# Kernel optimization log

Measured on AMD Instinct MI355X. Metric: run time of the kernel, lower is better.

## Reference

```python
import jax, jax.numpy as jnp
import numpy as np

N_EMBD = 1024
N_HEAD = 16  # per-source: this becomes the per-head DIM after the quirky view
B, T = 1, 2048


def setup_inputs() -> dict:
    key = jax.random.key(0)
    ks = jax.random.split(key, 5)
    s = 1.0 / np.sqrt(N_EMBD)
    x = jax.random.normal(ks[0], (B, T, N_EMBD), dtype=jnp.float32)
    attn_mask = jnp.ones((T, T), dtype=bool)
    W_qkv = jax.random.normal(ks[1], (N_EMBD, 3 * N_EMBD), dtype=jnp.float32) * s
    b_qkv = jnp.zeros((3 * N_EMBD,), dtype=jnp.float32)
    W_out = jax.random.normal(ks[2], (N_EMBD, N_EMBD), dtype=jnp.float32) * s
    b_out = jnp.zeros((N_EMBD,), dtype=jnp.float32)
    return {"x": x, "attn_mask": attn_mask, "W_qkv": W_qkv, "b_qkv": b_qkv,
            "W_out": W_out, "b_out": b_out}


def reference(x, attn_mask, W_qkv, b_qkv, W_out, b_out):
    Bb, Tt, C = x.shape
    H = N_HEAD            # per-head dim (source's layout quirk)
    nh = C // H           # number of heads = 64
    qkv = x @ W_qkv + b_qkv                      # [B,T,3C]
    q, k, v = jnp.split(qkv, 3, axis=-1)

    def to_heads(t):
        return t.reshape(Bb, Tt, nh, H).transpose(0, 2, 1, 3)  # [B,nh,T,H]

    q, k, v = to_heads(q), to_heads(k), to_heads(v)
    scale = 1.0 / np.sqrt(H)
    scores = jnp.einsum('bhqd,bhkd->bhqk', q, k) * scale       # [B,nh,T,T]
    causal = jnp.tril(jnp.ones((Tt, Tt), dtype=bool))
    scores = jnp.where(causal, scores, jnp.finfo(scores.dtype).min)
    p = jax.nn.softmax(scores, axis=-1)
    attn = jnp.einsum('bhqk,bhkd->bhqd', p, v)                 # [B,nh,T,H]
    attn = attn.transpose(0, 2, 1, 3).reshape(Bb, Tt, C)       # [B,T,C]
    return attn @ W_out + b_out
```

## Files before the change

kernel.cpp:

```cpp
#include <hip/hip_runtime.h>
#include <math.h>

#define T_SEQ 2048
#define C_EMB 1024
#define NH 64
#define HD 16

typedef __attribute__((ext_vector_type(4))) float    floatx4;
typedef __attribute__((ext_vector_type(4))) _Float16 halfx4;
typedef __attribute__((ext_vector_type(8))) _Float16 halfx8;

#if __has_builtin(__builtin_amdgcn_exp2f)
#define EXP2F(x) __builtin_amdgcn_exp2f(x)
#else
#define EXP2F(x) exp2f(x)
#endif

__device__ __forceinline__ void load_lds16(const void* g, void* l) {
    __builtin_amdgcn_global_load_lds(
        (const __attribute__((address_space(1))) unsigned int*)g,
        (__attribute__((address_space(3))) unsigned int*)l, 16, 0, 0);
}

__global__ __launch_bounds__(256) void prep_kernel(
    const float* __restrict__ x, const float* __restrict__ W_qkv,
    const float* __restrict__ W_out,
    _Float16* __restrict__ xb, _Float16* __restrict__ wqkvt,
    _Float16* __restrict__ woutt)
{
    __shared__ float s[32][33];
    const int b = blockIdx.x;
    const int t = threadIdx.x;

    if (b < 2048) {
        const int i = b * 256 + t;
        float4 v = ((const float4*)x)[i];
        halfx4 o = { (_Float16)v.x, (_Float16)v.y, (_Float16)v.z, (_Float16)v.w };
        ((halfx4*)xb)[i] = o;
        return;
    }

    const float* W; _Float16* Wt; int Kdim, Ndim, n0, k0;
    if (b < 5120) {
        const int bb = b - 2048;
        W = W_qkv; Wt = wqkvt; Kdim = 1024; Ndim = 3072;
        n0 = (bb % 96) * 32; k0 = (bb / 96) * 32;
    } else {
        const int bb = b - 5120;
        W = W_out; Wt = woutt; Kdim = 1024; Ndim = 1024;
        n0 = (bb & 31) * 32; k0 = (bb >> 5) * 32;
    }
    const int r  = t >> 3;
    const int c4 = (t & 7) * 4;
    float4 v = *(const float4*)&W[(size_t)(k0 + r) * Ndim + n0 + c4];
    s[r][c4 + 0] = v.x; s[r][c4 + 1] = v.y; s[r][c4 + 2] = v.z; s[r][c4 + 3] = v.w;
    __syncthreads();
    halfx4 o = { (_Float16)s[c4 + 0][r], (_Float16)s[c4 + 1][r],
                 (_Float16)s[c4 + 2][r], (_Float16)s[c4 + 3][r] };
    *(halfx4*)&Wt[(size_t)(n0 + r) * Kdim + k0 + c4] = o;
}

template <bool OUT_F16>
__global__ __launch_bounds__(256) void gemm_mfma_kernel(
    const _Float16* __restrict__ A,
    const _Float16* __restrict__ Bt,
    const float* __restrict__ bias,
    void* __restrict__ Cout,
    int M, int N, int K)
{
    __shared__ _Float16 As[2][64 * 32];
    __shared__ _Float16 Bs[2][128 * 32];

    const int tid = threadIdx.x;
    const int lane = tid & 63;
    const int w = tid >> 6;
    const int row0 = blockIdx.y * 64;
    const int col0 = blockIdx.x * 128;

    floatx4 acc[4][2] = {};

    const int lrow = lane >> 2;
    const int lko  = (lane & 3) * 8;
    const _Float16* agp = A  + (size_t)(row0 + w * 16 + lrow) * K + lko;
    const _Float16* bgp = Bt + (size_t)(col0 + w * 32 + lrow) * K + lko;
    const size_t rstep = (size_t)16 * K;

    const int kfr = (lane >> 4) * 8;
    const int fm = lane & 15;

    for (int k0 = 0; k0 < K; k0 += 64) {
#pragma unroll
        for (int s = 0; s < 2; ++s) {
            const int kk = k0 + s * 32;
            load_lds16(agp + kk,         &As[s][(w * 16) * 32]);
            load_lds16(bgp + kk,         &Bs[s][(w * 32) * 32]);
            load_lds16(bgp + kk + rstep, &Bs[s][(w * 32 + 16) * 32]);
        }
        __syncthreads();

#pragma unroll
        for (int s = 0; s < 2; ++s) {
            halfx8 af[4], bfv[2];
#pragma unroll
            for (int mi = 0; mi < 4; ++mi)
                af[mi] = *(const halfx8*)(&As[s][(mi * 16 + fm) * 32 + kfr]);
#pragma unroll
            for (int ni = 0; ni < 2; ++ni)
                bfv[ni] = *(const halfx8*)(&Bs[s][(w * 32 + ni * 16 + fm) * 32 + kfr]);

#pragma unroll
            for (int mi = 0; mi < 4; ++mi)
#pragma unroll
                for (int ni = 0; ni < 2; ++ni)
                    acc[mi][ni] = __builtin_amdgcn_mfma_f32_16x16x32_f16(
                        af[mi], bfv[ni], acc[mi][ni], 0, 0, 0);
        }
        __syncthreads();
    }

#pragma unroll
    for (int mi = 0; mi < 4; ++mi) {
        const int rm = row0 + mi * 16 + (lane >> 4) * 4;
#pragma unroll
        for (int ni = 0; ni < 2; ++ni) {
            const int cn = col0 + w * 32 + ni * 16 + fm;
            const float bv = bias[cn];
#pragma unroll
            for (int r = 0; r < 4; ++r) {
                float val = acc[mi][ni][r] + bv;
                if (OUT_F16)
                    ((_Float16*)Cout)[(size_t)(rm + r) * N + cn] = (_Float16)val;
                else
                    ((float*)Cout)[(size_t)(rm + r) * N + cn] = val;
            }
        }
    }
}

__global__ __launch_bounds__(512) void attn_mfma_kernel(
    const _Float16* __restrict__ qkv,
    _Float16* __restrict__ out)
{
    __shared__ _Float16 Ks[128 * 20];
    __shared__ _Float16 Vt[16 * 132];

    const int tid  = threadIdx.x;
    const int lane = tid & 63;
    const int w    = tid >> 6;
    const int quad = lane >> 4;
    const int ql   = lane & 15;
    const int h    = blockIdx.y;
    const int p    = blockIdx.x;

    const int q0s[2] = { p * 128 + w * 16, (15 - p) * 128 + w * 16 };
    const int nkt    = 16 - p;

    const _Float16 qscale = (_Float16)0.36067376f;
    halfx4 qf[2];
#pragma unroll
    for (int sub = 0; sub < 2; ++sub) {
        halfx4 qv = *(const halfx4*)(qkv + (size_t)(q0s[sub] + ql) * (3 * C_EMB)
                                     + h * HD + quad * 4);
#pragma unroll
        for (int j = 0; j < 4; ++j) qf[sub][j] = qv[j] * qscale;
    }

    const halfx4 onesA = { (_Float16)1.f, (_Float16)1.f, (_Float16)1.f, (_Float16)1.f };
    floatx4 o[2]  = {};
    floatx4 ol[2] = {};

    const int skp = tid >> 2;
    const int sdg = (tid & 3) * 4;

    for (int kt = 0; kt < nkt; ++kt) {
        const int kbase = kt * 128;
        {
            const _Float16* kp = qkv + (size_t)(kbase + skp) * (3 * C_EMB)
                                 + C_EMB + h * HD + sdg;
            *(halfx4*)&Ks[skp * 20 + sdg] = *(const halfx4*)kp;
            halfx4 vv = *(const halfx4*)(kp + C_EMB);
#pragma unroll
            for (int i = 0; i < 4; ++i) Vt[(sdg + i) * 132 + skp] = vv[i];
        }
        __syncthreads();

        halfx4 kf[8], vf[8];
#pragma unroll
        for (int st = 0; st < 8; ++st) {
            kf[st] = *(const halfx4*)&Ks[(st * 16 + ql) * 20 + quad * 4];
            vf[st] = *(const halfx4*)&Vt[ql * 132 + st * 16 + quad * 4];
        }

#pragma unroll
        for (int sub = 0; sub < 2; ++sub) {
            if (kbase > q0s[sub] + 15) continue;
            const bool need_mask = (kbase + 127 > q0s[sub]);

#pragma unroll
            for (int st = 0; st < 8; ++st) {
                floatx4 s = __builtin_amdgcn_mfma_f32_16x16x16f16(
                    kf[st], qf[sub], (floatx4){0.f, 0.f, 0.f, 0.f}, 0, 0, 0);
                if (need_mask) {
                    const int kg = kbase + st * 16 + quad * 4;
                    const int qg = q0s[sub] + ql;
#pragma unroll
                    for (int r = 0; r < 4; ++r)
                        if (kg + r > qg) s[r] = -INFINITY;
                }
                halfx4 pf;
#pragma unroll
                for (int r = 0; r < 4; ++r) pf[r] = (_Float16)EXP2F(s[r]);
                o[sub]  = __builtin_amdgcn_mfma_f32_16x16x16f16(
                    vf[st], pf, o[sub], 0, 0, 0);
                ol[sub] = __builtin_amdgcn_mfma_f32_16x16x16f16(
                    onesA, pf, ol[sub], 0, 0, 0);
            }
        }
        __syncthreads();
    }

#pragma unroll
    for (int sub = 0; sub < 2; ++sub) {
        const float inv_l = 1.f / ol[sub][0];
        halfx4 ov;
#pragma unroll
        for (int r = 0; r < 4; ++r) ov[r] = (_Float16)(o[sub][r] * inv_l);
        *(halfx4*)&out[(size_t)(q0s[sub] + ql) * C_EMB + h * HD + quad * 4] = ov;
    }
}

extern "C" void kernel_launch(void* const* d_in, const int* in_sizes, int n_in,
                              void* d_out, int out_size, void* d_ws, size_t ws_size,
                              hipStream_t stream) {
    const float* x     = (const float*)d_in[0];
    const float* W_qkv = (const float*)d_in[2];
    const float* b_qkv = (const float*)d_in[3];
    const float* W_out = (const float*)d_in[4];
    const float* b_out = (const float*)d_in[5];

    _Float16* xb    = (_Float16*)d_ws;
    _Float16* wqkvt = xb    + (size_t)T_SEQ * C_EMB;
    _Float16* woutt = wqkvt + (size_t)3 * C_EMB * C_EMB;
    _Float16* qkvb  = woutt + (size_t)C_EMB * C_EMB;
    _Float16* attnb = qkvb  + (size_t)T_SEQ * 3 * C_EMB;

    dim3 blk(256);

    prep_kernel<<<dim3(6144), blk, 0, stream>>>(x, W_qkv, W_out, xb, wqkvt, woutt);

    gemm_mfma_kernel<true><<<dim3(3 * C_EMB / 128, T_SEQ / 64), blk, 0, stream>>>(
        xb, wqkvt, b_qkv, qkvb, T_SEQ, 3 * C_EMB, C_EMB);

    attn_mfma_kernel<<<dim3(8, NH), dim3(512), 0, stream>>>(qkvb, attnb);

    gemm_mfma_kernel<false><<<dim3(C_EMB / 128, T_SEQ / 64), blk, 0, stream>>>(
        attnb, woutt, b_out, (float*)d_out, T_SEQ, C_EMB, C_EMB);
}
```

Measured before the change: 159.0 us.

## Double-buffer K/V tiles in attention and use 64x64 tiles for output GEMM

The attention kernel now keeps two K/V shared-memory buffers, loading the next tile while computing on the current one, so only one barrier per iteration is needed. The output projection switches to a new 64x64-tile GEMM kernel, doubling the block count from 256 to 512 to fill more compute units. In exchange the attention kernel uses twice the LDS, and the smaller GEMM tiles reuse each loaded operand less.

```diff
diff --git a/kernel.cpp b/kernel.cpp
--- a/kernel.cpp
+++ b/kernel.cpp
@@ -137,12 +137,82 @@
     }
 }
 
+__global__ __launch_bounds__(256) void gemm_mfma64_kernel(
+    const _Float16* __restrict__ A,
+    const _Float16* __restrict__ Bt,
+    const float* __restrict__ bias,
+    float* __restrict__ Cout,
+    int M, int N, int K)
+{
+    __shared__ _Float16 As[2][64 * 32];
+    __shared__ _Float16 Bs[2][64 * 32];
+
+    const int tid = threadIdx.x;
+    const int lane = tid & 63;
+    const int w = tid >> 6;
+    const int wm = w >> 1, wn = w & 1;
+    const int row0 = blockIdx.y * 64;
+    const int col0 = blockIdx.x * 64;
+
+    floatx4 acc[2][2] = {};
+
+    const int lrow = lane >> 2;
+    const int lko  = (lane & 3) * 8;
+    const _Float16* agp = A  + (size_t)(row0 + w * 16 + lrow) * K + lko;
+    const _Float16* bgp = Bt + (size_t)(col0 + w * 16 + lrow) * K + lko;
+
+    const int kfr = (lane >> 4) * 8;
+    const int fm = lane & 15;
+
+    for (int k0 = 0; k0 < K; k0 += 64) {
+#pragma unroll
+        for (int s = 0; s < 2; ++s) {
+            const int kk = k0 + s * 32;
+            load_lds16(agp + kk, &As[s][(w * 16) * 32]);
+            load_lds16(bgp + kk, &Bs[s][(w * 16) * 32]);
+        }
+        __syncthreads();
+
+#pragma unroll
+        for (int s = 0; s < 2; ++s) {
+            halfx8 af[2], bfv[2];
+#pragma unroll
+            for (int mi = 0; mi < 2; ++mi)
+                af[mi] = *(const halfx8*)(&As[s][(wm * 32 + mi * 16 + fm) * 32 + kfr]);
+#pragma unroll
+            for (int ni = 0; ni < 2; ++ni)
+                bfv[ni] = *(const halfx8*)(&Bs[s][(wn * 32 + ni * 16 + fm) * 32 + kfr]);
+
+#pragma unroll
+            for (int mi = 0; mi < 2; ++mi)
+#pragma unroll
+                for (int ni = 0; ni < 2; ++ni)
+                    acc[mi][ni] = __builtin_amdgcn_mfma_f32_16x16x32_f16(
+                        af[mi], bfv[ni], acc[mi][ni], 0, 0, 0);
+        }
+        __syncthreads();
+    }
+
+#pragma unroll
+    for (int mi = 0; mi < 2; ++mi) {
+        const int rm = row0 + wm * 32 + mi * 16 + (lane >> 4) * 4;
+#pragma unroll
+        for (int ni = 0; ni < 2; ++ni) {
+            const int cn = col0 + wn * 32 + ni * 16 + fm;
+            const float bv = bias[cn];
+#pragma unroll
+            for (int r = 0; r < 4; ++r)
+                Cout[(size_t)(rm + r) * N + cn] = acc[mi][ni][r] + bv;
+        }
+    }
+}
+
 __global__ __launch_bounds__(512) void attn_mfma_kernel(
     const _Float16* __restrict__ qkv,
     _Float16* __restrict__ out)
 {
-    __shared__ _Float16 Ks[128 * 20];
-    __shared__ _Float16 Vt[16 * 132];
+    __shared__ _Float16 Ks[2][128 * 20];
+    __shared__ _Float16 Vt[2][16 * 132];
 
     const int tid  = threadIdx.x;
     const int lane = tid & 63;
@@ -171,24 +241,34 @@
 
     const int skp = tid >> 2;
     const int sdg = (tid & 3) * 4;
+    const _Float16* kvbase = qkv + (size_t)skp * (3 * C_EMB) + C_EMB + h * HD + sdg;
+
+    {
+        const _Float16* kp = kvbase;
+        *(halfx4*)&Ks[0][skp * 20 + sdg] = *(const halfx4*)kp;
+        halfx4 vv = *(const halfx4*)(kp + C_EMB);
+#pragma unroll
+        for (int i = 0; i < 4; ++i) Vt[0][(sdg + i) * 132 + skp] = vv[i];
+    }
+    __syncthreads();
 
     for (int kt = 0; kt < nkt; ++kt) {
         const int kbase = kt * 128;
-        {
-            const _Float16* kp = qkv + (size_t)(kbase + skp) * (3 * C_EMB)
-                                 + C_EMB + h * HD + sdg;
-            *(halfx4*)&Ks[skp * 20 + sdg] = *(const halfx4*)kp;
+        const int cur = kt & 1, nxt = cur ^ 1;
+
+        if (kt + 1 < nkt) {
+            const _Float16* kp = kvbase + (size_t)(kbase + 128) * (3 * C_EMB);
+            *(halfx4*)&Ks[nxt][skp * 20 + sdg] = *(const halfx4*)kp;
             halfx4 vv = *(const halfx4*)(kp + C_EMB);
 #pragma unroll
-            for (int i = 0; i < 4; ++i) Vt[(sdg + i) * 132 + skp] = vv[i];
-        }
-        __syncthreads();
+            for (int i = 0; i < 4; ++i) Vt[nxt][(sdg + i) * 132 + skp] = vv[i];
+        }
 
         halfx4 kf[8], vf[8];
 #pragma unroll
         for (int st = 0; st < 8; ++st) {
-            kf[st] = *(const halfx4*)&Ks[(st * 16 + ql) * 20 + quad * 4];
-            vf[st] = *(const halfx4*)&Vt[ql * 132 + st * 16 + quad * 4];
+            kf[st] = *(const halfx4*)&Ks[cur][(st * 16 + ql) * 20 + quad * 4];
+            vf[st] = *(const halfx4*)&Vt[cur][ql * 132 + st * 16 + quad * 4];
         }
 
 #pragma unroll
@@ -253,6 +333,6 @@
 
     attn_mfma_kernel<<<dim3(8, NH), dim3(512), 0, stream>>>(qkvb, attnb);
 
-    gemm_mfma_kernel<false><<<dim3(C_EMB / 128, T_SEQ / 64), blk, 0, stream>>>(
+    gemm_mfma64_kernel<<<dim3(C_EMB / 64, T_SEQ / 64), blk, 0, stream>>>(
         attnb, woutt, b_out, (float*)d_out, T_SEQ, C_EMB, C_EMB);
 }
```

Result: faster. 153.6 us (median of 2 runs) (-3.4%).
